# Performance work log

Hardware: AMD Instinct MI355X
Metric: run time of the kernel (lower is better)

Reference implementation:

```python
import jax, jax.numpy as jnp
import numpy as np

# module config (matches init_kwargs)
H, W, C = 32, 32, 3
KH, KW, KC = 4, 4, 1
N_CLASS = 10
NBIN = 200
SHIFT = (0, 0)
NH, NW, NC = H // KH, W // KW, C // KC
NKERNEL = NH * NW * NC          # 192
NDIM_SUB = KH * KW * KC         # 16
NCOMP = NDIM_SUB                # n_component defaults to ndim_sub
NDIM = H * W * C                # 3072
NTRANS = NKERNEL * NCOMP        # 3072
N = 2048


def setup_inputs() -> dict:
    key = jax.random.key(0)
    k1, k2, k3, k4, k5, k6 = jax.random.split(key, 6)
    data = jax.random.normal(k1, (N, NDIM), dtype=jnp.float32)
    label = jax.random.randint(k2, (N,), 0, N_CLASS)
    # per-patch orthonormal projections: QR with sign fix, as in __init__
    wi = jax.random.normal(k3, (NKERNEL, NDIM_SUB, NCOMP), dtype=jnp.float32)
    Q, R = jnp.linalg.qr(wi)
    sign = jnp.sign(jnp.diagonal(R, axis1=-2, axis2=-1))
    wT_blocks = Q * sign[:, None, :]
    # monotone rational-quadratic spline knots per class / transformed dim
    dx = jax.random.uniform(k4, (N_CLASS, NTRANS, NBIN - 1), minval=0.5, maxval=1.5)
    dy = jax.random.uniform(k5, (N_CLASS, NTRANS, NBIN - 1), minval=0.5, maxval=1.5)
    z = jnp.zeros((N_CLASS, NTRANS, 1), jnp.float32)
    knots_x = -4.0 + 8.0 * jnp.concatenate([z, jnp.cumsum(dx, -1)], -1) / jnp.sum(dx, -1, keepdims=True)
    knots_y = -4.0 + 8.0 * jnp.concatenate([z, jnp.cumsum(dy, -1)], -1) / jnp.sum(dy, -1, keepdims=True)
    knots_d = jax.random.uniform(k6, (N_CLASS, NTRANS, NBIN), minval=0.5, maxval=1.5)
    return {"data": data, "label": label, "wT_blocks": wT_blocks,
            "knots_x": knots_x.astype(jnp.float32), "knots_y": knots_y.astype(jnp.float32),
            "knots_d": knots_d}


def construct_wT(wT_blocks):
    """Assemble block-structured (NDIM, NTRANS) projection from per-patch blocks."""
    dim = jnp.arange(NDIM).reshape(H, W, C)
    dim = jnp.roll(dim, (-SHIFT[0], -SHIFT[1]), axis=(0, 1))  # Shift() == negative roll
    # rows[b] = flat pixel indices of patch b; block order index = h*NW*NC + w*NC + c
    rows = dim.reshape(NH, KH, NW, KW, C).transpose(0, 2, 4, 1, 3).reshape(NKERNEL, NDIM_SUB)
    cols = jnp.arange(NKERNEL)[:, None] * NCOMP + jnp.arange(NCOMP)[None, :]
    wT = jnp.zeros((NDIM, NTRANS), wT_blocks.dtype)
    return wT.at[rows[:, :, None], cols[:, None, :]].set(wT_blocks)


def rq_spline(x, xx, yy, dd):
    """Monotone rational-quadratic spline with linear extrapolation.
    x: (N, T); xx/yy/dd: (T, K) knot positions / values / derivatives.
    Returns (y, log|dy/dx|), each (N, T)."""
    xT = x.T  # (T, N)
    lo, hi = xx[:, :1], xx[:, -1:]
    below, above = xT < lo, xT > hi
    xc = jnp.clip(xT, lo, hi)  # keep interior branch NaN-free
    k = jax.vmap(lambda kn, v: jnp.searchsorted(kn, v, side='right'))(xx, xc) - 1
    k = jnp.clip(k, 0, NBIN - 2)
    take = lambda a, i: jnp.take_along_axis(a, i, axis=1)
    xk, xk1 = take(xx, k), take(xx, k + 1)
    yk, yk1 = take(yy, k), take(yy, k + 1)
    dk, dk1 = take(dd, k), take(dd, k + 1)
    wdt = xk1 - xk
    s = (yk1 - yk) / wdt
    xi = (xc - xk) / wdt
    om = 1.0 - xi
    denom = s + (dk1 + dk - 2.0 * s) * xi * om
    ys = yk + (yk1 - yk) * (s * xi * xi + dk * xi * om) / denom
    lj_s = 2.0 * jnp.log(s) + jnp.log(dk1 * xi * xi + 2.0 * s * xi * om + dk * om * om) - 2.0 * jnp.log(denom)
    d0, dK = dd[:, :1], dd[:, -1:]
    y = jnp.where(below, yy[:, :1] + (xT - lo) * d0,
                  jnp.where(above, yy[:, -1:] + (xT - hi) * dK, ys))
    lj = jnp.where(below, jnp.log(d0), jnp.where(above, jnp.log(dK), lj_s))
    return y.T, lj.T


def reference(data, label, wT_blocks, knots_x, knots_y, knots_d):
    wT = construct_wT(wT_blocks)                 # (NDIM, NTRANS)
    data0 = data @ wT                            # (N, NTRANS)
    remaining = data - data0 @ wT.T              # orthogonal complement (zero here since full-rank)

    def body(carry, params):
        c, data1, logj = carry
        xx, yy, dd = params
        y, lj = rq_spline(data0, xx, yy, dd)
        m = label == c
        data1 = jnp.where(m[:, None], y, data1)
        logj = jnp.where(m, jnp.sum(lj, axis=1), logj)
        return (c + 1, data1, logj), None

    init = (jnp.int32(0), jnp.zeros_like(data0), jnp.zeros((data.shape[0],), data.dtype))
    (_, data1, logj), _ = jax.lax.scan(body, init, (knots_x, knots_y, knots_d))
    out = remaining + data1 @ wT.T
    return out, logj
```

## Files before the change

### kernel.cpp

```cpp
#include <hip/hip_runtime.h>

constexpr int NSAMP  = 2048;
constexpr int NDIM   = 3072;
constexpr int NTRANS = 3072;
constexpr int NBIN   = 200;
constexpr int NCLASS = 10;
constexpr int NPATCH = 192;
constexpr int BLK    = 256;
constexpr int DSTR   = 20;
constexpr int SA     = 4;
constexpr int SC     = 4;
constexpr int QP     = 48;
constexpr int QD     = 768;
constexpr int NL     = 128;
constexpr int LUTS   = 136;

__device__ __forceinline__ float4* xb_line(float* xb, int p, int sl) {
    return (float4*)(xb + ((size_t)p * NSAMP + (sl ^ (p & 63))) * 16);
}
__device__ __forceinline__ const float4* xb_line_c(const float* xb, int p, int sl) {
    return (const float4*)(xb + ((size_t)p * NSAMP + (sl ^ (p & 63))) * 16);
}

__global__ __launch_bounds__(1024)
void p0_prep(const int* __restrict__ label,
             int* __restrict__ slot,
             int* __restrict__ cls_off,
             float* __restrict__ logj_slot)
{
    __shared__ int s_lab[NSAMP];
    __shared__ int s_cnt[32][NCLASS];
    __shared__ int s_pre[32][NCLASS];
    __shared__ int s_tot[NCLASS];
    __shared__ int s_off[NCLASS + 1];
    const int tid  = threadIdx.x;
    const int lane = tid & 63;
    const int wv   = tid >> 6;

    for (int i = tid; i < NSAMP; i += 1024) {
        s_lab[i] = label[i];
        logj_slot[i] = 0.f;
    }
    __syncthreads();

    const unsigned long long ltmask = ((unsigned long long)1 << lane) - 1;
    int myrank[2], myc[2];
    #pragma unroll
    for (int pass = 0; pass < 2; ++pass) {
        const int n = pass * 1024 + tid;
        const int c = s_lab[n];
        myc[pass] = c;
        int r = 0;
        #pragma unroll
        for (int cls = 0; cls < NCLASS; ++cls) {
            const unsigned long long b = __ballot(c == cls);
            if (lane == 0) s_cnt[pass * 16 + wv][cls] = __popcll(b);
            if (cls == c)  r = __popcll(b & ltmask);
        }
        myrank[pass] = r;
    }
    __syncthreads();

    if (tid < 32 * NCLASS) {
        const int seg = tid & 31;
        const int cls = tid >> 5;
        int acc = 0;
        for (int s = 0; s < seg; ++s) acc += s_cnt[s][cls];
        s_pre[seg][cls] = acc;
        if (seg == 31) s_tot[cls] = acc + s_cnt[31][cls];
    }
    __syncthreads();
    if (tid == 0) {
        int a = 0;
        for (int c = 0; c < NCLASS; ++c) { s_off[c] = a; a += s_tot[c]; }
        s_off[NCLASS] = a;
    }
    __syncthreads();

    #pragma unroll
    for (int pass = 0; pass < 2; ++pass) {
        const int n   = pass * 1024 + tid;
        const int seg = pass * 16 + wv;
        const int c   = myc[pass];
        slot[n] = s_off[c] + s_pre[seg][c] + myrank[pass];
    }
    if (tid <= NCLASS) cls_off[tid] = s_off[tid];
}

__global__ __launch_bounds__(BLK, 4)
void pA_project(const float* __restrict__ data,
                const float* __restrict__ B,
                const int*   __restrict__ slot,
                float* __restrict__ xb)
{
    __shared__ float s_data[SA][NDIM];
    const int b   = blockIdx.x;
    const int tid = threadIdx.x;
    const int n0  = b * SA;

    #pragma unroll
    for (int s = 0; s < SA; ++s) {
        const float4* dr = (const float4*)(data + (size_t)(n0 + s) * NDIM);
        float4* sd = (float4*)s_data[s];
        #pragma unroll
        for (int j = 0; j < 3; ++j)
            sd[tid + BLK * j] = dr[tid + BLK * j];
    }
    int sls[SA];
    #pragma unroll
    for (int s = 0; s < SA; ++s) sls[s] = slot[n0 + s];
    __syncthreads();

    #pragma unroll 1
    for (int jj = 0; jj < 3; ++jj) {
        const int tau = tid + BLK * jj;
        const int p   = tau >> 2;
        const int q4  = tau & 3;
        const int nh  = p / 24;
        const int rem = p - nh * 24;
        const int nw  = rem / 3;
        const int ch  = rem - nw * 3;
        const int rowbase = nh * 384 + nw * 12 + ch;

        float4 Bp[16];
        const float4* Bg = (const float4*)(B + p * 256 + q4 * 4);
        #pragma unroll
        for (int i = 0; i < 16; ++i) Bp[i] = Bg[i * 4];

        #pragma unroll
        for (int s = 0; s < SA; ++s) {
            float dv[16];
            #pragma unroll
            for (int i = 0; i < 16; ++i)
                dv[i] = s_data[s][rowbase + (i >> 2) * 96 + (i & 3) * 3];

            float acc[4] = {0.f, 0.f, 0.f, 0.f};
            #pragma unroll
            for (int i = 0; i < 16; ++i) {
                acc[0] += Bp[i].x * dv[i];
                acc[1] += Bp[i].y * dv[i];
                acc[2] += Bp[i].z * dv[i];
                acc[3] += Bp[i].w * dv[i];
            }
            *(xb_line(xb, p, sls[s]) + q4) =
                make_float4(acc[0], acc[1], acc[2], acc[3]);
        }
    }
}

__global__ __launch_bounds__(BLK, 8)
void pB_spline(const float* __restrict__ kx,
               const float* __restrict__ ky,
               const float* __restrict__ kd,
               const int*   __restrict__ cls_off,
               float* __restrict__ xb,
               float* __restrict__ logj_slot)
{
    __shared__ float s_kx[16 * NBIN];
    __shared__ unsigned char s_lut[16 * LUTS];

    const int p   = blockIdx.x;
    const int c   = blockIdx.y;
    const int tid = threadIdx.x;
    const int t0  = p * 16;

    const size_t kofs = ((size_t)c * NTRANS + t0) * NBIN;
    const float4* gx = (const float4*)(kx + kofs);
    float4* lx = (float4*)s_kx;
    #pragma unroll 1
    for (int i = tid; i < 16 * NBIN / 4; i += BLK) lx[i] = gx[i];
    __syncthreads();

    {
        const int r  = tid >> 4;
        const int ch = tid & 15;
        const float* xx = s_kx + r * NBIN;
        const int j0 = ch * 8;
        const float xu0 = -4.0f + (float)j0 * (8.0f / NL);
        int klo = 0, khi = NBIN;
        #pragma unroll
        for (int it = 0; it < 8; ++it) {
            const int mid = (klo + khi) >> 1;
            const bool le = (xx[mid] <= xu0);
            klo = le ? mid : klo;
            khi = le ? khi : mid;
        }
        int k = klo;
        const int nj = (ch == 15) ? 9 : 8;
        unsigned char* lrow = s_lut + r * LUTS + j0;
        #pragma unroll 1
        for (int jj = 0; jj < nj; ++jj) {
            const float xuj = -4.0f + (float)(j0 + jj) * (8.0f / NL);
            while (k < NBIN - 1 && xx[k + 1] <= xuj) ++k;
            lrow[jj] = (unsigned char)k;
        }
    }
    __syncthreads();

    const int qq  = tid & 3;
    const int sid = tid >> 2;
    const float* sxx = s_kx + qq * 4 * NBIN;
    const float* kyp = ky + kofs + (size_t)(qq * 4) * NBIN;
    const float* kdp = kd + kofs + (size_t)(qq * 4) * NBIN;

    const int beg = cls_off[c];
    const int end = cls_off[c + 1];
    const int nit = (end - beg + 63) >> 6;

    int sl = beg + sid;
    float4 v = make_float4(0.f, 0.f, 0.f, 0.f);
    float4* lcur = nullptr;
    if (sl < end) { lcur = xb_line(xb, p, sl) + qq; v = *lcur; }

    #pragma unroll 1
    for (int it = 0; it < nit; ++it) {
        const int sln = sl + 64;
        float4 vn = make_float4(0.f, 0.f, 0.f, 0.f);
        float4* lnx = nullptr;
        if (it + 1 < nit && sln < end) { lnx = xb_line(xb, p, sln) + qq; vn = *lnx; }

        if (lcur) {
            float xs[4] = {v.x, v.y, v.z, v.w};
            float lj_sum = 0.f;
            #pragma unroll
            for (int j = 0; j < 4; ++j) {
                const float* xx  = sxx + j * NBIN;
                const float* yyg = kyp + j * NBIN;
                const float* ddg = kdp + j * NBIN;
                const unsigned char* lrow = s_lut + (qq * 4 + j) * LUTS;
                const float x  = xs[j];
                const float lo = xx[0];
                const float hi = xx[NBIN - 1];

                float y, lj;
                if (x < lo) {
                    const float d0 = ddg[0];
                    y  = yyg[0] + (x - lo) * d0;
                    lj = __logf(d0);
                } else if (x > hi) {
                    const float dK = ddg[NBIN - 1];
                    y  = yyg[NBIN - 1] + (x - hi) * dK;
                    lj = __logf(dK);
                } else {
                    int u = (int)((x + 4.0f) * (NL / 8.0f));
                    u = u < 0 ? 0 : (u > NL - 1 ? NL - 1 : u);
                    int klo = (int)lrow[u] - 1;
                    klo = klo < 0 ? 0 : klo;
                    int khi = (int)lrow[u + 1] + 2;
                    khi = khi > NBIN ? NBIN : khi;
                    #pragma unroll
                    for (int itb = 0; itb < 3; ++itb) {
                        const int mid = (klo + khi) >> 1;
                        const bool le = (xx[mid] <= x);
                        klo = le ? mid : klo;
                        khi = le ? khi : mid;
                    }
                    int k = klo;
                    if (k > NBIN - 2) k = NBIN - 2;

                    const float xk = xx[k], xk1 = xx[k + 1];
                    const float yk = yyg[k], yk1 = yyg[k + 1];
                    const float dk = ddg[k], dk1 = ddg[k + 1];

                    const float wdt     = xk1 - xk;
                    const float inv_wdt = __fdividef(1.f, wdt);
                    const float dy      = yk1 - yk;
                    const float s       = dy * inv_wdt;
                    const float xi      = (x - xk) * inv_wdt;
                    const float om      = 1.f - xi;
                    const float denom   = s + (dk1 + dk - 2.f * s) * xi * om;
                    const float r       = __fdividef(1.f, denom);
                    const float num     = dy * (s * xi * xi + dk * xi * om);
                    y = yk + num * r;
                    const float Nq = dk1 * xi * xi + 2.f * s * xi * om + dk * om * om;
                    const float t2 = s * r;
                    lj = __logf(t2 * t2 * Nq);
                }
                xs[j] = y - x;
                lj_sum += lj;
            }

            *lcur = make_float4(xs[0], xs[1], xs[2], xs[3]);

            lj_sum += __shfl_xor(lj_sum, 1);
            lj_sum += __shfl_xor(lj_sum, 2);
            if (qq == 0) atomicAdd(&logj_slot[sl], lj_sum);
        }

        sl = sln; lcur = lnx; v = vn;
    }
}

__global__ __launch_bounds__(BLK, 8)
void pC_recon(const float* __restrict__ data,
              const float* __restrict__ B,
              const int*   __restrict__ slot,
              const float* __restrict__ xb,
              const float* __restrict__ logj_slot,
              float* __restrict__ out,
              float* __restrict__ logj)
{
    __shared__ float s_diff[SC][QP * DSTR];
    const int g   = blockIdx.x;
    const int qtr = blockIdx.y;
    const int tid = threadIdx.x;
    const int n0  = g * SC;
    const int pq  = qtr * QP;

    int sls[SC];
    #pragma unroll
    for (int s = 0; s < SC; ++s) sls[s] = slot[n0 + s];

    #pragma unroll
    for (int jj = 0; jj < 3; ++jj) {
        const int e  = tid + BLK * jj;
        const int s  = e / (QP * 4);
        const int r  = e - s * (QP * 4);
        const int pl = r >> 2;
        const int q  = r & 3;
        const float4 v = *(xb_line_c(xb, pq + pl, sls[s]) + q);
        *(float4*)&s_diff[s][pl * DSTR + q * 4] = v;
    }
    if (qtr == 0 && tid < SC) logj[n0 + tid] = logj_slot[sls[tid]];
    __syncthreads();

    #pragma unroll 1
    for (int j = 0; j < QD / BLK; ++j) {
        const int d  = qtr * QD + tid + BLK * j;
        const int ch = d % 3;
        const int hw = d / 3;
        const int w  = hw & 31;
        const int h  = hw >> 5;
        const int p  = ((h >> 2) * 8 + (w >> 2)) * 3 + ch;
        const int pl = p - pq;
        const int i  = (h & 3) * 4 + (w & 3);

        const float4* Bp4 = (const float4*)(B + p * 256 + i * 16);
        const float4 b0 = Bp4[0], b1 = Bp4[1], b2 = Bp4[2], b3 = Bp4[3];

        #pragma unroll
        for (int s = 0; s < SC; ++s) {
            const float4* dp4 = (const float4*)&s_diff[s][pl * DSTR];
            const float4 d0 = dp4[0], d1 = dp4[1], d2 = dp4[2], d3 = dp4[3];
            float acc = data[(size_t)(n0 + s) * NDIM + d];
            acc += b0.x * d0.x + b0.y * d0.y + b0.z * d0.z + b0.w * d0.w;
            acc += b1.x * d1.x + b1.y * d1.y + b1.z * d1.z + b1.w * d1.w;
            acc += b2.x * d2.x + b2.y * d2.y + b2.z * d2.z + b2.w * d2.w;
            acc += b3.x * d3.x + b3.y * d3.y + b3.z * d3.z + b3.w * d3.w;
            out[(size_t)(n0 + s) * NDIM + d] = acc;
        }
    }
}

extern "C" void kernel_launch(void* const* d_in, const int* in_sizes, int n_in,
                              void* d_out, int out_size, void* d_ws, size_t ws_size,
                              hipStream_t stream) {
    const float* data  = (const float*)d_in[0];
    const int*   label = (const int*)  d_in[1];
    const float* B     = (const float*)d_in[2];
    const float* kx    = (const float*)d_in[3];
    const float* ky    = (const float*)d_in[4];
    const float* kd    = (const float*)d_in[5];

    float* out  = (float*)d_out;
    float* logj = (float*)d_out + (size_t)NSAMP * NDIM;

    char* ws = (char*)d_ws;
    size_t off = 0;
    float* xb        = (float*)(ws + off); off += (size_t)NPATCH * NSAMP * 16 * 4;
    float* logj_slot = (float*)(ws + off); off += NSAMP * 4;
    int*   slot      = (int*)  (ws + off); off += NSAMP * 4;
    int*   cls_off   = (int*)  (ws + off); off += 64;

    p0_prep   <<<1, 1024, 0, stream>>>(label, slot, cls_off, logj_slot);
    pA_project<<<NSAMP / SA, BLK, 0, stream>>>(data, B, slot, xb);
    dim3 gridB(NPATCH, NCLASS);
    pB_spline <<<gridB, BLK, 0, stream>>>(kx, ky, kd, cls_off, xb, logj_slot);
    dim3 gridC(NSAMP / SC, NDIM / QD);
    pC_recon  <<<gridC, BLK, 0, stream>>>(data, B, slot, xb, logj_slot, out, logj);
}
```

Before: 198.3 us.

## Split projection and spline kernels into two grid halves for more parallelism

The projection kernel now runs a second grid dimension that handles half of the input pixels (patch rows 0–3 or 4–7) per block. This halves its shared-memory tile, which should allow more resident blocks, though its inner loop now leaves half the threads idle on its second pass. The spline kernel adds a z dimension that splits each class's sample range in two across separate blocks. That raises block count and shortens per-block serial loops, but each block duplicates the knot load and lookup-table build.

```diff
diff --git a/kernel.cpp b/kernel.cpp
--- a/kernel.cpp
+++ b/kernel.cpp
@@ -9,6 +9,8 @@
 constexpr int BLK    = 256;
 constexpr int DSTR   = 20;
 constexpr int SA     = 4;
+constexpr int HD     = 1536;
+constexpr int HP     = 96;
 constexpr int SC     = 4;
 constexpr int QP     = 48;
 constexpr int QD     = 768;
@@ -93,18 +95,19 @@
                 const int*   __restrict__ slot,
                 float* __restrict__ xb)
 {
-    __shared__ float s_data[SA][NDIM];
+    __shared__ float s_data[SA][HD];
     const int b   = blockIdx.x;
+    const int z   = blockIdx.y;
     const int tid = threadIdx.x;
     const int n0  = b * SA;
+    const int dof = z * HD;
 
     #pragma unroll
     for (int s = 0; s < SA; ++s) {
-        const float4* dr = (const float4*)(data + (size_t)(n0 + s) * NDIM);
+        const float4* dr = (const float4*)(data + (size_t)(n0 + s) * NDIM + dof);
         float4* sd = (float4*)s_data[s];
-        #pragma unroll
-        for (int j = 0; j < 3; ++j)
-            sd[tid + BLK * j] = dr[tid + BLK * j];
+        sd[tid] = dr[tid];
+        if (tid < HD / 4 - BLK) sd[tid + BLK] = dr[tid + BLK];
     }
     int sls[SA];
     #pragma unroll
@@ -112,15 +115,14 @@
     __syncthreads();
 
     #pragma unroll 1
-    for (int jj = 0; jj < 3; ++jj) {
-        const int tau = tid + BLK * jj;
-        const int p   = tau >> 2;
-        const int q4  = tau & 3;
+    for (int e = tid; e < HP * 4; e += BLK) {
+        const int p   = z * HP + (e >> 2);
+        const int q4  = e & 3;
         const int nh  = p / 24;
         const int rem = p - nh * 24;
         const int nw  = rem / 3;
         const int ch  = rem - nw * 3;
-        const int rowbase = nh * 384 + nw * 12 + ch;
+        const int rowbase = nh * 384 + nw * 12 + ch - dof;
 
         float4 Bp[16];
         const float4* Bg = (const float4*)(B + p * 256 + q4 * 4);
@@ -161,6 +163,7 @@
 
     const int p   = blockIdx.x;
     const int c   = blockIdx.y;
+    const int zz  = blockIdx.z;
     const int tid = threadIdx.x;
     const int t0  = p * 16;
 
@@ -203,9 +206,12 @@
     const float* kyp = ky + kofs + (size_t)(qq * 4) * NBIN;
     const float* kdp = kd + kofs + (size_t)(qq * 4) * NBIN;
 
-    const int beg = cls_off[c];
-    const int end = cls_off[c + 1];
-    const int nit = (end - beg + 63) >> 6;
+    const int beg0 = cls_off[c];
+    const int end0 = cls_off[c + 1];
+    const int h0   = (end0 - beg0 + 1) >> 1;
+    const int beg  = beg0 + zz * h0;
+    const int end  = zz ? end0 : beg0 + h0;
+    const int nit  = (end - beg + 63) >> 6;
 
     int sl = beg + sid;
     float4 v = make_float4(0.f, 0.f, 0.f, 0.f);
@@ -373,8 +379,9 @@
     int*   cls_off   = (int*)  (ws + off); off += 64;
 
     p0_prep   <<<1, 1024, 0, stream>>>(label, slot, cls_off, logj_slot);
-    pA_project<<<NSAMP / SA, BLK, 0, stream>>>(data, B, slot, xb);
-    dim3 gridB(NPATCH, NCLASS);
+    dim3 gridA(NSAMP / SA, 2);
+    pA_project<<<gridA, BLK, 0, stream>>>(data, B, slot, xb);
+    dim3 gridB(NPATCH, NCLASS, 2);
     pB_spline <<<gridB, BLK, 0, stream>>>(kx, ky, kd, cls_off, xb, logj_slot);
     dim3 gridC(NSAMP / SC, NDIM / QD);
     pC_recon  <<<gridC, BLK, 0, stream>>>(data, B, slot, xb, logj_slot, out, logj);
```

Result: slower. 207.0 us (+4.4%).
